# Kernel optimization log

Hardware: AMD Instinct MI355X
Metric: run time of the kernel (lower is better)

Reference implementation:

```python
import jax, jax.numpy as jnp
import numpy as np

B, N, E = 8, 50000, 800000
IN_DIM, OUT_DIM = 64, 64


def setup_inputs() -> dict:
    key = jax.random.key(0)
    k_x, k_src, k_dst, k_ws, k_bs, k_wn, k_bn = jax.random.split(key, 7)
    x = jax.random.normal(k_x, (B, N, IN_DIM), dtype=jnp.float32)
    src = jax.random.randint(k_src, (E,), 0, N, dtype=jnp.int64)
    dst = jax.random.randint(k_dst, (E,), 0, N, dtype=jnp.int64)
    edge_index = jnp.stack([src, dst], axis=1)  # (E, 2)
    # nn.Linear init: U(-1/sqrt(in_dim), 1/sqrt(in_dim))
    bound = 1.0 / np.sqrt(IN_DIM)
    W_self = jax.random.uniform(k_ws, (OUT_DIM, IN_DIM), jnp.float32, -bound, bound)
    b_self = jax.random.uniform(k_bs, (OUT_DIM,), jnp.float32, -bound, bound)
    W_neigh = jax.random.uniform(k_wn, (OUT_DIM, IN_DIM), jnp.float32, -bound, bound)
    b_neigh = jax.random.uniform(k_bn, (OUT_DIM,), jnp.float32, -bound, bound)
    return {"x": x, "edge_index": edge_index, "W_self": W_self, "b_self": b_self,
            "W_neigh": W_neigh, "b_neigh": b_neigh}


def reference(x, edge_index, W_self, b_self, W_neigh, b_neigh):
    # x: (B, N, D); edge_index: (E, 2) [src, dst], shared topology across batch
    src = edge_index[:, 0]
    dst = edge_index[:, 1]
    # scatter-add neighbor aggregation, vectorized over batch
    agg = jnp.zeros_like(x).at[:, dst].add(x[:, src])  # (B, N, D)
    h_self = jnp.einsum('bnd,od->bno', x, W_self) + b_self
    h_neigh = jnp.einsum('bnd,od->bno', agg, W_neigh) + b_neigh
    return jax.nn.relu(h_self + h_neigh)
```

## Files before the change

kernel.cpp:

```cpp
#include <hip/hip_runtime.h>

#define Bn 8
#define Nn 50000
#define En 800000
#define Dd 64
#define CAP 64

typedef __attribute__((ext_vector_type(8))) unsigned short ushort8;
typedef __attribute__((ext_vector_type(8))) __bf16 bf16x8;
typedef __attribute__((ext_vector_type(4))) float floatx4;

__device__ __forceinline__ unsigned short f2bf(float f) {
  unsigned int u = __builtin_bit_cast(unsigned int, f);
  u = (u + 0x7FFFu + ((u >> 16) & 1u)) >> 16;
  return (unsigned short)u;
}

__device__ __forceinline__ int swz(int row, int byte_in_row) {
  return (row * 256 + byte_in_row) ^ ((row & 7) << 4);
}

__global__ __launch_bounds__(256) void k_fconv(const float* __restrict__ x,
                                               unsigned short* __restrict__ xb,
                                               const int* __restrict__ ei,
                                               int* __restrict__ deg,
                                               unsigned short* __restrict__ bucket) {
  const size_t gid = (size_t)blockIdx.x * 256 + threadIdx.x;
  const size_t i = gid * 4;
  const float4 v = *(const float4*)(x + i);
  ushort4 o;
  o.x = f2bf(v.x); o.y = f2bf(v.y); o.z = f2bf(v.z); o.w = f2bf(v.w);
  *(ushort4*)(xb + i) = o;
  if (gid < En) {
    const int2 e = *(const int2*)(ei + 2 * gid);
    const int p = atomicAdd(&deg[e.y], 1);
    if (p < CAP) bucket[(e.y << 6) + p] = (unsigned short)e.x;
  }
}

__global__ __launch_bounds__(256, 5) void k_main(
    const unsigned short* __restrict__ xb, const unsigned short* __restrict__ bucket,
    const int* __restrict__ deg, const float* __restrict__ Ws,
    const float* __restrict__ bs, const float* __restrict__ Wn,
    const float* __restrict__ bn, float* __restrict__ out) {
  __shared__ __align__(16) unsigned short Wt[64 * 128];
  __shared__ __align__(16) unsigned short A[64 * 128];

  const int tid = threadIdx.x;
  const int b = blockIdx.x & 7;
  const int node0 = (blockIdx.x >> 3) * 64;
  const int wave = tid >> 6;
  const int lane = tid & 63;
  char* Ac = (char*)A;
  char* Wc = (char*)Wt;

  for (int i = tid; i < 64 * 32; i += 256) {
    const int o = i >> 5;
    const int k = (i & 31) * 4;
    const float4 wv = (k < 64) ? *(const float4*)(Ws + o * 64 + k)
                               : *(const float4*)(Wn + o * 64 + (k - 64));
    ushort4 u;
    u.x = f2bf(wv.x); u.y = f2bf(wv.y); u.z = f2bf(wv.z); u.w = f2bf(wv.w);
    *(ushort4*)(Wc + swz(o, k * 2)) = u;
  }

  const int slot = lane >> 3;
  const int li = lane & 7;
  const size_t xb_base = (size_t)b * Nn * Dd + (size_t)(li * 8);

  for (int g = 0; g < 2; ++g) {
    const int nl = wave * 16 + g * 8 + slot;
    const int node = node0 + nl;
    float acc[8] = {0.f, 0.f, 0.f, 0.f, 0.f, 0.f, 0.f, 0.f};
    if (node < Nn) {
      const uint4 sv = *(const uint4*)(xb + xb_base + (size_t)node * Dd);
      const int cnt = min(deg[node], CAP);
      const unsigned short* bkt = bucket + (node << 6);
      const int nch = (cnt + 7) >> 3;
      for (int c = 0; c < nch; ++c) {
        const uint4 e = *(const uint4*)(bkt + c * 8);
        const unsigned int ew[4] = {e.x, e.y, e.z, e.w};
        #pragma unroll
        for (int t = 0; t < 8; ++t) {
          unsigned int s = (ew[t >> 1] >> ((t & 1) * 16)) & 0xFFFFu;
          const float m = (s < (unsigned)Nn) ? 1.0f : 0.0f;
          s = min(s, (unsigned)(Nn - 1));
          const uint4 v = *(const uint4*)(xb + xb_base + (size_t)s * Dd);
          const unsigned int w[4] = {v.x, v.y, v.z, v.w};
          #pragma unroll
          for (int j = 0; j < 4; ++j) {
            acc[2 * j]     = fmaf(m, __builtin_bit_cast(float, w[j] << 16), acc[2 * j]);
            acc[2 * j + 1] = fmaf(m, __builtin_bit_cast(float, w[j] & 0xFFFF0000u), acc[2 * j + 1]);
          }
        }
      }
      *(uint4*)(Ac + swz(nl, li * 16)) = sv;
    } else {
      *(uint4*)(Ac + swz(nl, li * 16)) = make_uint4(0, 0, 0, 0);
    }
    ushort8 av;
    #pragma unroll
    for (int j = 0; j < 8; ++j) av[j] = f2bf(acc[j]);
    *(ushort8*)(Ac + swz(nl, 128 + li * 16)) = av;
  }
  __syncthreads();

  const int col = lane & 15;
  const int quad = lane >> 4;
  bf16x8 af[4];
  {
    const int row = wave * 16 + col;
    #pragma unroll
    for (int k = 0; k < 4; ++k)
      af[k] = __builtin_bit_cast(bf16x8, *(const ushort8*)(Ac + swz(row, quad * 16 + k * 64)));
  }
  #pragma unroll
  for (int t = 0; t < 4; ++t) {
    floatx4 acc = {0.f, 0.f, 0.f, 0.f};
    const int row = t * 16 + col;
    #pragma unroll
    for (int k = 0; k < 4; ++k) {
      bf16x8 bf = __builtin_bit_cast(bf16x8, *(const ushort8*)(Wc + swz(row, quad * 16 + k * 64)));
      acc = __builtin_amdgcn_mfma_f32_16x16x32_bf16(af[k], bf, acc, 0, 0, 0);
    }
    const int o = t * 16 + col;
    const float bv = bs[o] + bn[o];
    #pragma unroll
    for (int r = 0; r < 4; ++r) {
      const int node = node0 + wave * 16 + quad * 4 + r;
      if (node < Nn) {
        float v = acc[r] + bv;
        out[((size_t)b * Nn + node) * Dd + o] = v > 0.f ? v : 0.f;
      }
    }
  }
}

#define OFF_XB 0ull
#define OFF_DEG 51200000ull
#define OFF_BKT 51400000ull
#define WS_NEED 57800000ull

extern "C" void kernel_launch(void* const* d_in, const int* in_sizes, int n_in,
                              void* d_out, int out_size, void* d_ws,
                              size_t ws_size, hipStream_t stream) {
  const float* x = (const float*)d_in[0];
  const int* ei = (const int*)d_in[1];
  const float* Ws = (const float*)d_in[2];
  const float* bs = (const float*)d_in[3];
  const float* Wn = (const float*)d_in[4];
  const float* bn = (const float*)d_in[5];
  float* out = (float*)d_out;

  if (ws_size < WS_NEED) return;

  char* ws = (char*)d_ws;
  unsigned short* xb = (unsigned short*)(ws + OFF_XB);
  int* deg = (int*)(ws + OFF_DEG);
  unsigned short* bucket = (unsigned short*)(ws + OFF_BKT);

  hipMemsetAsync(deg, 0, Nn * sizeof(int), stream);
  hipMemsetAsync(bucket, 0xFF, (size_t)Nn * CAP * sizeof(unsigned short), stream);
  k_fconv<<<(Bn * Nn * Dd / 4) / 256, 256, 0, stream>>>(x, xb, ei, deg, bucket);
  const int ntiles = (Nn + 63) / 64;
  k_main<<<ntiles * Bn, 256, 0, stream>>>(xb, bucket, deg, Ws, bs, Wn, bn, out);
}
```

Before: 328.9 us.

## Prepack bf16 weight fragments globally and drop per-block LDS weight staging

The conversion kernel now converts W_self and W_neigh to bf16 once, stores them in the exact MFMA B-fragment lane order, and precomputes the summed bias. The main kernel reads weight fragments straight from global memory (cache-resident) instead of every block converting and swizzling a 64x128 weight tile into LDS. That tile is removed, which halves shared memory per block, so the occupancy hint goes from 5 to 8 blocks and the block barrier is dropped, since each wave only reads the A rows it wrote itself. Edge bucketing is also spread to every eighth thread across the whole grid rather than the first 800k threads, which distributes the atomics. The cost is extra global or L2 traffic for weight fragments in the MFMA loop, and more register pressure under the tighter launch bound.

```diff
diff --git a/kernel.cpp b/kernel.cpp
--- a/kernel.cpp
+++ b/kernel.cpp
@@ -24,26 +24,44 @@
                                                unsigned short* __restrict__ xb,
                                                const int* __restrict__ ei,
                                                int* __restrict__ deg,
-                                               unsigned short* __restrict__ bucket) {
+                                               unsigned short* __restrict__ bucket,
+                                               const float* __restrict__ Ws,
+                                               const float* __restrict__ Wn,
+                                               const float* __restrict__ bs,
+                                               const float* __restrict__ bn,
+                                               unsigned short* __restrict__ Wb,
+                                               float* __restrict__ bb) {
   const size_t gid = (size_t)blockIdx.x * 256 + threadIdx.x;
   const size_t i = gid * 4;
   const float4 v = *(const float4*)(x + i);
   ushort4 o;
   o.x = f2bf(v.x); o.y = f2bf(v.y); o.z = f2bf(v.z); o.w = f2bf(v.w);
   *(ushort4*)(xb + i) = o;
-  if (gid < En) {
-    const int2 e = *(const int2*)(ei + 2 * gid);
-    const int p = atomicAdd(&deg[e.y], 1);
-    if (p < CAP) bucket[(e.y << 6) + p] = (unsigned short)e.x;
+  if ((gid & 7) == 0) {
+    const size_t e = gid >> 3;
+    const int2 ep = *(const int2*)(ei + 2 * e);
+    const int p = atomicAdd(&deg[ep.y], 1);
+    if (p < CAP) bucket[((size_t)ep.y << 6) + p] = (unsigned short)ep.x;
   }
+  if (gid < 1024) {
+    const int f = (int)gid >> 6, ln = (int)gid & 63;
+    const int t = f >> 2, k = f & 3;
+    const int col = ln & 15, quad = ln >> 4;
+    const int orow = t * 16 + col;
+    const int kd = k * 32 + quad * 8;
+    const float* wsrc = (kd < 64) ? (Ws + orow * 64 + kd) : (Wn + orow * 64 + (kd - 64));
+    ushort8 u;
+    #pragma unroll
+    for (int j = 0; j < 8; ++j) u[j] = f2bf(wsrc[j]);
+    *(ushort8*)(Wb + gid * 8) = u;
+  }
+  if (gid < 64) bb[gid] = bs[gid] + bn[gid];
 }
 
-__global__ __launch_bounds__(256, 5) void k_main(
+__global__ __launch_bounds__(256, 8) void k_main(
     const unsigned short* __restrict__ xb, const unsigned short* __restrict__ bucket,
-    const int* __restrict__ deg, const float* __restrict__ Ws,
-    const float* __restrict__ bs, const float* __restrict__ Wn,
-    const float* __restrict__ bn, float* __restrict__ out) {
-  __shared__ __align__(16) unsigned short Wt[64 * 128];
+    const int* __restrict__ deg, const unsigned short* __restrict__ Wb,
+    const float* __restrict__ bb, float* __restrict__ out) {
   __shared__ __align__(16) unsigned short A[64 * 128];
 
   const int tid = threadIdx.x;
@@ -52,17 +70,6 @@
   const int wave = tid >> 6;
   const int lane = tid & 63;
   char* Ac = (char*)A;
-  char* Wc = (char*)Wt;
-
-  for (int i = tid; i < 64 * 32; i += 256) {
-    const int o = i >> 5;
-    const int k = (i & 31) * 4;
-    const float4 wv = (k < 64) ? *(const float4*)(Ws + o * 64 + k)
-                               : *(const float4*)(Wn + o * 64 + (k - 64));
-    ushort4 u;
-    u.x = f2bf(wv.x); u.y = f2bf(wv.y); u.z = f2bf(wv.z); u.w = f2bf(wv.w);
-    *(ushort4*)(Wc + swz(o, k * 2)) = u;
-  }
 
   const int slot = lane >> 3;
   const int li = lane & 7;
@@ -103,7 +110,6 @@
     for (int j = 0; j < 8; ++j) av[j] = f2bf(acc[j]);
     *(ushort8*)(Ac + swz(nl, 128 + li * 16)) = av;
   }
-  __syncthreads();
 
   const int col = lane & 15;
   const int quad = lane >> 4;
@@ -117,20 +123,18 @@
   #pragma unroll
   for (int t = 0; t < 4; ++t) {
     floatx4 acc = {0.f, 0.f, 0.f, 0.f};
-    const int row = t * 16 + col;
     #pragma unroll
     for (int k = 0; k < 4; ++k) {
-      bf16x8 bf = __builtin_bit_cast(bf16x8, *(const ushort8*)(Wc + swz(row, quad * 16 + k * 64)));
+      bf16x8 bf = __builtin_bit_cast(bf16x8, *(const ushort8*)(Wb + ((t * 4 + k) * 64 + lane) * 8));
       acc = __builtin_amdgcn_mfma_f32_16x16x32_bf16(af[k], bf, acc, 0, 0, 0);
     }
-    const int o = t * 16 + col;
-    const float bv = bs[o] + bn[o];
+    const float bv = bb[t * 16 + col];
     #pragma unroll
     for (int r = 0; r < 4; ++r) {
       const int node = node0 + wave * 16 + quad * 4 + r;
       if (node < Nn) {
         float v = acc[r] + bv;
-        out[((size_t)b * Nn + node) * Dd + o] = v > 0.f ? v : 0.f;
+        out[((size_t)b * Nn + node) * Dd + t * 16 + col] = v > 0.f ? v : 0.f;
       }
     }
   }
@@ -139,7 +143,9 @@
 #define OFF_XB 0ull
 #define OFF_DEG 51200000ull
 #define OFF_BKT 51400000ull
-#define WS_NEED 57800000ull
+#define OFF_WB 57800000ull
+#define OFF_BB 57816384ull
+#define WS_NEED 57816640ull
 
 extern "C" void kernel_launch(void* const* d_in, const int* in_sizes, int n_in,
                               void* d_out, int out_size, void* d_ws,
@@ -158,10 +164,12 @@
   unsigned short* xb = (unsigned short*)(ws + OFF_XB);
   int* deg = (int*)(ws + OFF_DEG);
   unsigned short* bucket = (unsigned short*)(ws + OFF_BKT);
+  unsigned short* Wb = (unsigned short*)(ws + OFF_WB);
+  float* bb = (float*)(ws + OFF_BB);
 
   hipMemsetAsync(deg, 0, Nn * sizeof(int), stream);
   hipMemsetAsync(bucket, 0xFF, (size_t)Nn * CAP * sizeof(unsigned short), stream);
-  k_fconv<<<(Bn * Nn * Dd / 4) / 256, 256, 0, stream>>>(x, xb, ei, deg, bucket);
+  k_fconv<<<(Bn * Nn * Dd / 4) / 256, 256, 0, stream>>>(x, xb, ei, deg, bucket, Ws, Wn, bs, bn, Wb, bb);
   const int ntiles = (Nn + 63) / 64;
-  k_main<<<ntiles * Bn, 256, 0, stream>>>(xb, bucket, deg, Ws, bs, Wn, bn, out);
+  k_main<<<ntiles * Bn, 256, 0, stream>>>(xb, bucket, deg, Wb, bb, out);
 }
```

Measured after the change: 344.2 us. +4.6%, slower.
